# Optimization experiments

Hardware: AMD Instinct MI355X
Metric: run time of the kernel (lower is better)

Reference implementation:

```python
import jax, jax.numpy as jnp
import numpy as np

B, N, T = 8, 512, 24
HID, HOR, NID, NBLOCKS, NHIDL = 256, 24, 64, 3, 2  # block_layers=3 -> 1 input layer + 2 hidden
D = T + N * T + NID  # FcBlock input size = 12376


def div_no_nan(a, b):
    safe = jnp.where(b == 0, jnp.ones_like(b), b)
    return jnp.where(b == 0, jnp.zeros_like(a), a / safe)


def setup_inputs() -> dict:
    key = jax.random.key(0)
    ks = jax.random.split(key, 16)
    s_in = 1.0 / np.sqrt(D)
    s_h = 1.0 / np.sqrt(HID)
    return {
        "history_in": jax.random.uniform(ks[0], (B, N, T), jnp.float32),
        "node_id_in": jax.random.randint(ks[1], (B, N, 1), 0, N, dtype=jnp.int32),
        "time_of_day_in": jax.random.uniform(ks[2], (B, N, 1), jnp.float32),
        "adjacency_in": jax.random.uniform(ks[3], (B, N, N), jnp.float32),
        "node_emb": jax.random.uniform(ks[4], (N, NID), jnp.float32, -0.05, 0.05),
        "W_in": jax.random.normal(ks[5], (NBLOCKS, D, HID), jnp.float32) * s_in,
        "b_in": jnp.zeros((NBLOCKS, HID), jnp.float32),
        "W_hid": jax.random.normal(ks[6], (NBLOCKS, NHIDL, HID, HID), jnp.float32) * s_h,
        "b_hid": jnp.zeros((NBLOCKS, NHIDL, HID), jnp.float32),
        "W_f": jax.random.normal(ks[7], (NBLOCKS, HID, HOR), jnp.float32) * s_h,
        "b_f": jnp.zeros((NBLOCKS, HOR), jnp.float32),
        "W_b": jax.random.normal(ks[8], (NBLOCKS, HID, D), jnp.float32) * s_h,
        "b_b": jnp.zeros((NBLOCKS, D), jnp.float32),
    }


def fc_block(x, W_in, b_in, W_hid, b_hid, W_f, b_f, W_b, b_b):
    # x: [B, N, D]
    h = jax.nn.relu(jnp.einsum('bnd,dh->bnh', x, W_in) + b_in)
    for l in range(NHIDL):
        h = jax.nn.relu(jnp.einsum('bnh,hk->bnk', h, W_hid[l]) + b_hid[l])
    forecast = jnp.einsum('bnh,ho->bno', h, W_f) + b_f
    backcast = jax.nn.relu(x - (jnp.einsum('bnh,hd->bnd', h, W_b) + b_b))
    return backcast, forecast


def reference(history_in, node_id_in, time_of_day_in, adjacency_in, node_emb,
              W_in, b_in, W_hid, b_hid, W_f, b_f, W_b, b_b):
    # node id embedding: [B,N,1] -> [B,N,1,NID] -> squeeze -> [B,N,NID]
    node_id = node_emb[node_id_in[..., 0]]

    # use_time_gate=False: time_gate_forward = 0, time_gate_backward = 0
    # history_in = history_in / (1 + 0) -> unchanged

    # graph_layer_type == 'none' branch with graph_adj = adjacency_in [B,N,N]
    level = jnp.max(history_in, axis=-1, keepdims=True)          # [B,N,1]
    history = div_no_nan(history_in, level)                      # [B,N,T]

    # tile history to all pairs and weight by adjacency: [B,N,N,T]
    all_node_history = adjacency_in[..., None] * history_in[:, None, :, :]
    all_node_history = all_node_history.reshape(B, N, N * T)     # [B,N,N*T]
    all_node_history = div_no_nan(all_node_history - level, level)
    all_node_history = jnp.where(all_node_history > 0, all_node_history, 0.0)

    history = jnp.concatenate([history, all_node_history, node_id], axis=-1)  # [B,N,D]

    backcast, forecast_out = fc_block(history, W_in[0], b_in[0], W_hid[0], b_hid[0],
                                      W_f[0], b_f[0], W_b[0], b_b[0])
    for i in range(1, NBLOCKS):
        backcast, fb = fc_block(backcast, W_in[i], b_in[i], W_hid[i], b_hid[i],
                                W_f[i], b_f[i], W_b[i], b_b[i])
        forecast_out = forecast_out + fb

    forecast_out = forecast_out[:, :, :HOR]
    forecast = forecast_out * level  # (1 + time_gate_forward) = 1
    return backcast, forecast
```

## Files before the change

### kernel.cpp

```cpp
#include <hip/hip_runtime.h>

#define Bq   8
#define Nn   512
#define Tt   24
#define NIDc 64
#define HIDc 256
#define HORc 24
#define Dd   12376
#define Mm   4096
#define DdPad 12384
#define NbPad 12416
#define SPLITK 8
#define KCHUNK 1568

typedef float  f32x4  __attribute__((ext_vector_type(4)));
typedef short  bf16x8 __attribute__((ext_vector_type(8)));

__device__ __forceinline__ ushort f2bf(float f) {
    unsigned u = __float_as_uint(f);
    u += 0x7FFF + ((u >> 16) & 1);
    return (ushort)(u >> 16);
}
__device__ __forceinline__ float bf2f(ushort h) {
    return __uint_as_float(((unsigned)h) << 16);
}

#define ASYNC16(g, l) __builtin_amdgcn_global_load_lds(                        \
    (const __attribute__((address_space(1))) unsigned*)(g),                    \
    (__attribute__((address_space(3))) unsigned*)(l), 16, 0, 0)

__global__ __launch_bounds__(256) void build_x_kernel(
    const float* __restrict__ hist, const int* __restrict__ nid,
    const float* __restrict__ adj, const float* __restrict__ emb,
    ushort* __restrict__ x, float* __restrict__ level)
{
    int bn = blockIdx.x;
    int b  = bn >> 9;
    __shared__ float sh[Tt];
    __shared__ float slv;
    int tid = threadIdx.x;
    const float* hrow = hist + (size_t)bn * Tt;
    if (tid < Tt) sh[tid] = hrow[tid];
    __syncthreads();
    if (tid == 0) {
        float m = sh[0];
        #pragma unroll
        for (int t = 1; t < Tt; t++) m = fmaxf(m, sh[t]);
        slv = m;
        level[bn] = m;
    }
    __syncthreads();
    float lv  = slv;
    float inv = (lv == 0.0f) ? 0.0f : 1.0f / lv;
    ushort* xr = x + (size_t)bn * DdPad;
    if (tid < Tt) xr[tid] = f2bf(sh[tid] * inv);
    const float* hb   = hist + (size_t)b * Nn * Tt;
    const float* arow = adj  + (size_t)bn * Nn;
    for (int base = tid * 8; base < Nn * Tt; base += 256 * 8) {
        bf16x8 pack;
        #pragma unroll
        for (int e = 0; e < 8; e++) {
            int idx = base + e;
            int m_ = idx / Tt;
            int t  = idx - m_ * Tt;
            float v = arow[m_] * hb[m_ * Tt + t];
            float r = (v - lv) * inv;
            pack[e] = (short)f2bf((r > 0.0f) ? r : 0.0f);
        }
        *(bf16x8*)(xr + Tt + base) = pack;
    }
    if (tid < NIDc) {
        int id = nid[bn];
        xr[Tt + Nn * Tt + tid] = f2bf(emb[(size_t)id * NIDc + tid]);
    }
    if (tid < DdPad - Dd) xr[Dd + tid] = 0;
}

__global__ __launch_bounds__(256) void transpose_w(
    const float* __restrict__ W, ushort* __restrict__ Bt,
    int K, int N, int Kpad)
{
    __shared__ ushort tile[32][72];
    const int k0 = blockIdx.x * 32;
    const int n0 = blockIdx.y * 64;
    const int tid = threadIdx.x;
    #pragma unroll
    for (int i = 0; i < 8; i++) {
        const int idx = tid + i * 256;
        const int kk = idx >> 6;
        const int nn = idx & 63;
        const int gk = k0 + kk, gn = n0 + nn;
        const float v = (gk < K && gn < N) ? W[(size_t)gk * N + gn] : 0.0f;
        tile[kk][nn] = f2bf(v);
    }
    __syncthreads();
    const int n  = tid >> 2;
    const int kc = (tid & 3) << 3;
    uint4 o;
    o.x = (unsigned)tile[kc + 0][n] | ((unsigned)tile[kc + 1][n] << 16);
    o.y = (unsigned)tile[kc + 2][n] | ((unsigned)tile[kc + 3][n] << 16);
    o.z = (unsigned)tile[kc + 4][n] | ((unsigned)tile[kc + 5][n] << 16);
    o.w = (unsigned)tile[kc + 6][n] | ((unsigned)tile[kc + 7][n] << 16);
    *(uint4*)(Bt + (size_t)(n0 + n) * Kpad + k0 + kc) = o;
}

template <int TM, int TN, int EPI>
__global__ __launch_bounds__(256) void gemm_mfma(
    const ushort* __restrict__ A, int lda,
    const ushort* __restrict__ Bt, int ldbt,
    const float* __restrict__ bias,
    const ushort* __restrict__ X, int ldx,
    void* __restrict__ Cp, int ldc,
    int K, int N, int chunk)
{
    constexpr int WI = TM / 32;
    constexpr int WJ = TN / 32;
    __shared__ ushort As[TM * 32];
    __shared__ ushort Bs[TN * 32];

    const int tid  = threadIdx.x;
    const int row0 = blockIdx.x * TM;
    const int col0 = blockIdx.y * TN;
    const int spl  = blockIdx.z;
    const int kstart = spl * chunk;
    const int kend   = min(K, kstart + chunk);
    const int iters  = (kend - kstart) >> 5;

    const int lane = tid & 63;
    const int wave = tid >> 6;
    const int quad = lane >> 4;
    const int l15  = lane & 15;
    const int wm   = (wave >> 1) * (TM / 2);
    const int wn   = (wave & 1) * (TN / 2);

    f32x4 acc[WI][WJ];
    #pragma unroll
    for (int i = 0; i < WI; i++)
        #pragma unroll
        for (int j = 0; j < WJ; j++)
            acc[i][j] = (f32x4){0.f, 0.f, 0.f, 0.f};

    for (int kt = 0; kt < iters; ++kt) {
        const int kb = kstart + (kt << 5);
        #pragma unroll
        for (int s = wave; s < TM / 16; s += 4) {
            const int r = s * 16 + (lane >> 2);
            ASYNC16(A + (size_t)(row0 + r) * lda + kb + ((lane & 3) << 3),
                    As + s * 512);
        }
        #pragma unroll
        for (int s = wave; s < TN / 16; s += 4) {
            const int r = s * 16 + (lane >> 2);
            ASYNC16(Bt + (size_t)(col0 + r) * ldbt + kb + ((lane & 3) << 3),
                    Bs + s * 512);
        }
        __syncthreads();

        bf16x8 af[WI], bfr[WJ];
        #pragma unroll
        for (int i = 0; i < WI; i++)
            af[i] = *(const bf16x8*)&As[(wm + i * 16 + l15) * 32 + quad * 8];
        #pragma unroll
        for (int j = 0; j < WJ; j++)
            bfr[j] = *(const bf16x8*)&Bs[(wn + j * 16 + l15) * 32 + quad * 8];
        #pragma unroll
        for (int i = 0; i < WI; i++)
            #pragma unroll
            for (int j = 0; j < WJ; j++)
                acc[i][j] = __builtin_amdgcn_mfma_f32_16x16x32_bf16(
                    bfr[j], af[i], acc[i][j], 0, 0, 0);
        __syncthreads();
    }

    #pragma unroll
    for (int i = 0; i < WI; i++) {
        const int row = row0 + wm + i * 16 + l15;
        #pragma unroll
        for (int j = 0; j < WJ; j++) {
            const int c0 = col0 + wn + j * 16 + quad * 4;
            const f32x4 v = acc[i][j];
            if (EPI == 0) {
                *(f32x4*)&((float*)Cp)[(size_t)spl * Mm * HIDc +
                                       (size_t)row * ldc + c0] = v;
            } else if (EPI == 1) {
                const float4 bb = *(const float4*)&bias[c0];
                ushort4 o;
                o.x = f2bf(fmaxf(v[0] + bb.x, 0.f));
                o.y = f2bf(fmaxf(v[1] + bb.y, 0.f));
                o.z = f2bf(fmaxf(v[2] + bb.z, 0.f));
                o.w = f2bf(fmaxf(v[3] + bb.w, 0.f));
                *(ushort4*)&((ushort*)Cp)[(size_t)row * ldc + c0] = o;
            } else if (EPI == 2) {
                if (c0 < N) {
                    const float4 bb = *(const float4*)&bias[c0];
                    const ushort4 xq = *(const ushort4*)&X[(size_t)row * ldx + c0];
                    f32x4 o;
                    o[0] = fmaxf(bf2f(xq.x) - (v[0] + bb.x), 0.f);
                    o[1] = fmaxf(bf2f(xq.y) - (v[1] + bb.y), 0.f);
                    o[2] = fmaxf(bf2f(xq.z) - (v[2] + bb.z), 0.f);
                    o[3] = fmaxf(bf2f(xq.w) - (v[3] + bb.w), 0.f);
                    __builtin_nontemporal_store(
                        o, (f32x4*)&((float*)Cp)[(size_t)row * ldc + c0]);
                }
            } else {
                if (c0 < N) {
                    const float4 bb = *(const float4*)&bias[c0];
                    const ushort4 xq = *(const ushort4*)&X[(size_t)row * ldx + c0];
                    ushort4 o;
                    o.x = f2bf(fmaxf(bf2f(xq.x) - (v[0] + bb.x), 0.f));
                    o.y = f2bf(fmaxf(bf2f(xq.y) - (v[1] + bb.y), 0.f));
                    o.z = f2bf(fmaxf(bf2f(xq.z) - (v[2] + bb.z), 0.f));
                    o.w = f2bf(fmaxf(bf2f(xq.w) - (v[3] + bb.w), 0.f));
                    *(ushort4*)&((ushort*)Cp)[(size_t)row * ldc + c0] = o;
                }
            }
        }
    }
}

__global__ __launch_bounds__(256) void reduce_hin(
    const float* __restrict__ partial, const float* __restrict__ bias,
    ushort* __restrict__ h)
{
    const int gid = (blockIdx.x * 256 + threadIdx.x) * 4;
    f32x4 s = *(const f32x4*)&bias[gid & (HIDc - 1)];
    #pragma unroll
    for (int j = 0; j < SPLITK; j++)
        s += *(const f32x4*)&partial[(size_t)j * (Mm * HIDc) + gid];
    ushort4 o;
    o.x = f2bf(fmaxf(s[0], 0.f));
    o.y = f2bf(fmaxf(s[1], 0.f));
    o.z = f2bf(fmaxf(s[2], 0.f));
    o.w = f2bf(fmaxf(s[3], 0.f));
    *(ushort4*)&h[gid] = o;
}

__global__ __launch_bounds__(256) void gemm_forecast_kernel(
    const ushort* __restrict__ h, const float* __restrict__ Wf,
    const float* __restrict__ bf, float* __restrict__ fc, int accumulate)
{
    int gid = blockIdx.x * 256 + threadIdx.x;
    if (gid >= Mm * HORc) return;
    int row = gid / HORc;
    int col = gid - row * HORc;
    const ushort* hr = h + (size_t)row * HIDc;
    float acc = 0.0f;
    #pragma unroll 4
    for (int k = 0; k < HIDc; k++)
        acc = fmaf(bf2f(hr[k]), Wf[k * HORc + col], acc);
    acc += bf[col];
    if (accumulate) fc[gid] += acc;
    else            fc[gid]  = acc;
}

__global__ __launch_bounds__(256) void finalize_kernel(
    const float* __restrict__ fc, const float* __restrict__ level,
    float* __restrict__ out)
{
    int gid = blockIdx.x * 256 + threadIdx.x;
    if (gid >= Mm * HORc) return;
    out[gid] = fc[gid] * level[gid / HORc];
}

extern "C" void kernel_launch(void* const* d_in, const int* in_sizes, int n_in,
                              void* d_out, int out_size, void* d_ws, size_t ws_size,
                              hipStream_t stream)
{
    const float* hist  = (const float*)d_in[0];
    const int*   nid   = (const int*)  d_in[1];
    const float* adj   = (const float*)d_in[3];
    const float* emb   = (const float*)d_in[4];
    const float* W_in  = (const float*)d_in[5];
    const float* b_in  = (const float*)d_in[6];
    const float* W_hid = (const float*)d_in[7];
    const float* b_hid = (const float*)d_in[8];
    const float* W_f   = (const float*)d_in[9];
    const float* b_f   = (const float*)d_in[10];
    const float* W_b   = (const float*)d_in[11];
    const float* b_b   = (const float*)d_in[12];

    float* bout = (float*)d_out;
    float* fout = (float*)d_out + (size_t)Mm * Dd;

    char* ws = (char*)d_ws;
    size_t off = 0;
    float*  level = (float*) (ws + off); off += 16384;
    float*  fc    = (float*) (ws + off); off += (size_t)Mm * HORc * 4;
    ushort* hA    = (ushort*)(ws + off); off += (size_t)Mm * HIDc * 2;
    ushort* hB    = (ushort*)(ws + off); off += (size_t)Mm * HIDc * 2;
    ushort* WtIn  = (ushort*)(ws + off); off += (size_t)3 * HIDc * DdPad * 2;
    ushort* WtHid = (ushort*)(ws + off); off += (size_t)6 * HIDc * HIDc * 2;
    ushort* WtB   = (ushort*)(ws + off); off += (size_t)3 * NbPad * HIDc * 2;
    float*  part  = (float*) (ws + off); off += (size_t)SPLITK * Mm * HIDc * 4;
    ushort* xb    = (ushort*)(ws + off); off += (size_t)Mm * DdPad * 2;

    build_x_kernel<<<Mm, 256, 0, stream>>>(hist, nid, adj, emb, xb, level);

    for (int i = 0; i < 3; i++)
        transpose_w<<<dim3(DdPad / 32, HIDc / 64), 256, 0, stream>>>(
            W_in + (size_t)i * Dd * HIDc, WtIn + (size_t)i * HIDc * DdPad,
            Dd, HIDc, DdPad);
    for (int l = 0; l < 6; l++)
        transpose_w<<<dim3(HIDc / 32, HIDc / 64), 256, 0, stream>>>(
            W_hid + (size_t)l * HIDc * HIDc, WtHid + (size_t)l * HIDc * HIDc,
            HIDc, HIDc, HIDc);
    for (int i = 0; i < 3; i++)
        transpose_w<<<dim3(HIDc / 32, NbPad / 64), 256, 0, stream>>>(
            W_b + (size_t)i * HIDc * Dd, WtB + (size_t)i * NbPad * HIDc,
            HIDc, Dd, HIDc);

    for (int i = 0; i < 3; i++) {
        const float* bi  = b_in  + (size_t)i * HIDc;
        const float* bh0 = b_hid + (size_t)(i * 2 + 0) * HIDc;
        const float* bh1 = b_hid + (size_t)(i * 2 + 1) * HIDc;
        const float* Wfi = W_f   + (size_t)i * HIDc * HORc;
        const float* bfi = b_f   + (size_t)i * HORc;
        const float* bbi = b_b   + (size_t)i * Dd;

        gemm_mfma<128, 128, 0>
            <<<dim3(Mm / 128, HIDc / 128, SPLITK), 256, 0, stream>>>(
            xb, DdPad, WtIn + (size_t)i * HIDc * DdPad, DdPad,
            nullptr, nullptr, 0, part, HIDc, DdPad, HIDc, KCHUNK);
        reduce_hin<<<Mm * HIDc / 1024, 256, 0, stream>>>(part, bi, hA);

        gemm_mfma<64, 64, 1>
            <<<dim3(Mm / 64, HIDc / 64, 1), 256, 0, stream>>>(
            hA, HIDc, WtHid + (size_t)(2 * i) * HIDc * HIDc, HIDc,
            bh0, nullptr, 0, hB, HIDc, HIDc, HIDc, HIDc);
        gemm_mfma<64, 64, 1>
            <<<dim3(Mm / 64, HIDc / 64, 1), 256, 0, stream>>>(
            hB, HIDc, WtHid + (size_t)(2 * i + 1) * HIDc * HIDc, HIDc,
            bh1, nullptr, 0, hA, HIDc, HIDc, HIDc, HIDc);

        gemm_forecast_kernel<<<(Mm * HORc + 255) / 256, 256, 0, stream>>>(
            hA, Wfi, bfi, fc, i > 0 ? 1 : 0);

        if (i < 2) {
            gemm_mfma<128, 128, 3>
                <<<dim3(Mm / 128, NbPad / 128, 1), 256, 0, stream>>>(
                hA, HIDc, WtB + (size_t)i * NbPad * HIDc, HIDc,
                bbi, xb, DdPad, xb, DdPad, HIDc, Dd, HIDc);
        } else {
            gemm_mfma<128, 128, 2>
                <<<dim3(Mm / 128, NbPad / 128, 1), 256, 0, stream>>>(
                hA, HIDc, WtB + (size_t)i * NbPad * HIDc, HIDc,
                bbi, xb, DdPad, bout, Dd, HIDc, Dd, HIDc);
        }
    }

    finalize_kernel<<<(Mm * HORc + 255) / 256, 256, 0, stream>>>(fc, level, fout);
}
```

Measured before the change: 935.1 us.

## Double-buffer LDS tiles in MFMA GEMM, prefetch epilogue operands, shrink hidden tiles

Shared-memory A/B tiles are double-buffered: the next K-slice is loaded asynchronously while MFMAs run on the current one. Explicit vmcnt waits and raw s_barriers replace the two __syncthreads per iteration. Bias and residual X values for the epilogue are loaded before the main loop, so their latency overlaps the K loop, at the cost of extra registers. The hidden-layer GEMMs switch from 64x64 to 32x32 tiles for more blocks, and the final backcast store no longer uses a nontemporal hint.

```diff
diff --git a/kernel.cpp b/kernel.cpp
--- a/kernel.cpp
+++ b/kernel.cpp
@@ -115,8 +115,13 @@
 {
     constexpr int WI = TM / 32;
     constexpr int WJ = TN / 32;
-    __shared__ ushort As[TM * 32];
-    __shared__ ushort Bs[TN * 32];
+    constexpr int SA = TM / 16;
+    constexpr int SB = TN / 16;
+    constexpr int LPW = (SA + SB) / 4;
+    static_assert((SA + SB) % 4 == 0, "uniform loads per wave required");
+    static_assert(LPW == 1 || LPW == 2 || LPW == 4, "vmcnt literal");
+    __shared__ ushort As[2][TM * 32];
+    __shared__ ushort Bs[2][TN * 32];
 
     const int tid  = threadIdx.x;
     const int row0 = blockIdx.x * TM;
@@ -140,36 +145,85 @@
         for (int j = 0; j < WJ; j++)
             acc[i][j] = (f32x4){0.f, 0.f, 0.f, 0.f};
 
+    auto stage = [&](int buf, int kb) {
+        #pragma unroll
+        for (int t = 0; t < LPW; t++) {
+            const int s = wave + 4 * t;
+            if (s < SA) {
+                const int r = s * 16 + (lane >> 2);
+                ASYNC16(A + (size_t)(row0 + r) * lda + kb + ((lane & 3) << 3),
+                        &As[buf][s * 512]);
+            } else {
+                const int s2 = s - SA;
+                const int r = s2 * 16 + (lane >> 2);
+                ASYNC16(Bt + (size_t)(col0 + r) * ldbt + kb + ((lane & 3) << 3),
+                        &Bs[buf][s2 * 512]);
+            }
+        }
+    };
+
+    stage(0, kstart);
+
+    float4  bpre[WJ];
+    ushort4 xpre[WI][WJ];
+    bool    cok[WJ];
+    #pragma unroll
+    for (int j = 0; j < WJ; j++) {
+        const int c0 = col0 + wn + j * 16 + quad * 4;
+        cok[j] = (c0 < N);
+        if constexpr (EPI == 1) {
+            bpre[j] = *(const float4*)&bias[c0];
+        } else if constexpr (EPI >= 2) {
+            bpre[j] = cok[j] ? *(const float4*)&bias[c0]
+                             : float4{0.f, 0.f, 0.f, 0.f};
+        }
+    }
+    if constexpr (EPI >= 2) {
+        #pragma unroll
+        for (int i = 0; i < WI; i++) {
+            const int row = row0 + wm + i * 16 + l15;
+            #pragma unroll
+            for (int j = 0; j < WJ; j++) {
+                const int c0 = col0 + wn + j * 16 + quad * 4;
+                xpre[i][j] = cok[j]
+                    ? *(const ushort4*)&X[(size_t)row * ldx + c0]
+                    : ushort4{0, 0, 0, 0};
+            }
+        }
+    }
+
     for (int kt = 0; kt < iters; ++kt) {
-        const int kb = kstart + (kt << 5);
-        #pragma unroll
-        for (int s = wave; s < TM / 16; s += 4) {
-            const int r = s * 16 + (lane >> 2);
-            ASYNC16(A + (size_t)(row0 + r) * lda + kb + ((lane & 3) << 3),
-                    As + s * 512);
-        }
-        #pragma unroll
-        for (int s = wave; s < TN / 16; s += 4) {
-            const int r = s * 16 + (lane >> 2);
-            ASYNC16(Bt + (size_t)(col0 + r) * ldbt + kb + ((lane & 3) << 3),
-                    Bs + s * 512);
-        }
-        __syncthreads();
+        const int cur = kt & 1;
+        if (kt + 1 < iters) {
+            stage(cur ^ 1, kstart + ((kt + 1) << 5));
+            if constexpr (LPW == 4)
+                asm volatile("s_waitcnt vmcnt(4)" ::: "memory");
+            else if constexpr (LPW == 2)
+                asm volatile("s_waitcnt vmcnt(2)" ::: "memory");
+            else
+                asm volatile("s_waitcnt vmcnt(1)" ::: "memory");
+        } else {
+            asm volatile("s_waitcnt vmcnt(0)" ::: "memory");
+        }
+        __builtin_amdgcn_s_barrier();
+        __builtin_amdgcn_sched_barrier(0);
 
         bf16x8 af[WI], bfr[WJ];
         #pragma unroll
         for (int i = 0; i < WI; i++)
-            af[i] = *(const bf16x8*)&As[(wm + i * 16 + l15) * 32 + quad * 8];
+            af[i] = *(const bf16x8*)&As[cur][(wm + i * 16 + l15) * 32 + quad * 8];
         #pragma unroll
         for (int j = 0; j < WJ; j++)
-            bfr[j] = *(const bf16x8*)&Bs[(wn + j * 16 + l15) * 32 + quad * 8];
+            bfr[j] = *(const bf16x8*)&Bs[cur][(wn + j * 16 + l15) * 32 + quad * 8];
         #pragma unroll
         for (int i = 0; i < WI; i++)
             #pragma unroll
             for (int j = 0; j < WJ; j++)
                 acc[i][j] = __builtin_amdgcn_mfma_f32_16x16x32_bf16(
                     bfr[j], af[i], acc[i][j], 0, 0, 0);
-        __syncthreads();
+
+        __builtin_amdgcn_sched_barrier(0);
+        __builtin_amdgcn_s_barrier();
     }
 
     #pragma unroll
@@ -179,38 +233,32 @@
         for (int j = 0; j < WJ; j++) {
             const int c0 = col0 + wn + j * 16 + quad * 4;
             const f32x4 v = acc[i][j];
-            if (EPI == 0) {
+            if constexpr (EPI == 0) {
                 *(f32x4*)&((float*)Cp)[(size_t)spl * Mm * HIDc +
                                        (size_t)row * ldc + c0] = v;
-            } else if (EPI == 1) {
-                const float4 bb = *(const float4*)&bias[c0];
+            } else if constexpr (EPI == 1) {
                 ushort4 o;
-                o.x = f2bf(fmaxf(v[0] + bb.x, 0.f));
-                o.y = f2bf(fmaxf(v[1] + bb.y, 0.f));
-                o.z = f2bf(fmaxf(v[2] + bb.z, 0.f));
-                o.w = f2bf(fmaxf(v[3] + bb.w, 0.f));
+                o.x = f2bf(fmaxf(v[0] + bpre[j].x, 0.f));
+                o.y = f2bf(fmaxf(v[1] + bpre[j].y, 0.f));
+                o.z = f2bf(fmaxf(v[2] + bpre[j].z, 0.f));
+                o.w = f2bf(fmaxf(v[3] + bpre[j].w, 0.f));
                 *(ushort4*)&((ushort*)Cp)[(size_t)row * ldc + c0] = o;
-            } else if (EPI == 2) {
-                if (c0 < N) {
-                    const float4 bb = *(const float4*)&bias[c0];
-                    const ushort4 xq = *(const ushort4*)&X[(size_t)row * ldx + c0];
+            } else if constexpr (EPI == 2) {
+                if (cok[j]) {
                     f32x4 o;
-                    o[0] = fmaxf(bf2f(xq.x) - (v[0] + bb.x), 0.f);
-                    o[1] = fmaxf(bf2f(xq.y) - (v[1] + bb.y), 0.f);
-                    o[2] = fmaxf(bf2f(xq.z) - (v[2] + bb.z), 0.f);
-                    o[3] = fmaxf(bf2f(xq.w) - (v[3] + bb.w), 0.f);
-                    __builtin_nontemporal_store(
-                        o, (f32x4*)&((float*)Cp)[(size_t)row * ldc + c0]);
+                    o[0] = fmaxf(bf2f(xpre[i][j].x) - (v[0] + bpre[j].x), 0.f);
+                    o[1] = fmaxf(bf2f(xpre[i][j].y) - (v[1] + bpre[j].y), 0.f);
+                    o[2] = fmaxf(bf2f(xpre[i][j].z) - (v[2] + bpre[j].z), 0.f);
+                    o[3] = fmaxf(bf2f(xpre[i][j].w) - (v[3] + bpre[j].w), 0.f);
+                    *(f32x4*)&((float*)Cp)[(size_t)row * ldc + c0] = o;
                 }
             } else {
-                if (c0 < N) {
-                    const float4 bb = *(const float4*)&bias[c0];
-                    const ushort4 xq = *(const ushort4*)&X[(size_t)row * ldx + c0];
+                if (cok[j]) {
                     ushort4 o;
-                    o.x = f2bf(fmaxf(bf2f(xq.x) - (v[0] + bb.x), 0.f));
-                    o.y = f2bf(fmaxf(bf2f(xq.y) - (v[1] + bb.y), 0.f));
-                    o.z = f2bf(fmaxf(bf2f(xq.z) - (v[2] + bb.z), 0.f));
-                    o.w = f2bf(fmaxf(bf2f(xq.w) - (v[3] + bb.w), 0.f));
+                    o.x = f2bf(fmaxf(bf2f(xpre[i][j].x) - (v[0] + bpre[j].x), 0.f));
+                    o.y = f2bf(fmaxf(bf2f(xpre[i][j].y) - (v[1] + bpre[j].y), 0.f));
+                    o.z = f2bf(fmaxf(bf2f(xpre[i][j].z) - (v[2] + bpre[j].z), 0.f));
+                    o.w = f2bf(fmaxf(bf2f(xpre[i][j].w) - (v[3] + bpre[j].w), 0.f));
                     *(ushort4*)&((ushort*)Cp)[(size_t)row * ldc + c0] = o;
                 }
             }
@@ -323,12 +371,12 @@
             nullptr, nullptr, 0, part, HIDc, DdPad, HIDc, KCHUNK);
         reduce_hin<<<Mm * HIDc / 1024, 256, 0, stream>>>(part, bi, hA);
 
-        gemm_mfma<64, 64, 1>
-            <<<dim3(Mm / 64, HIDc / 64, 1), 256, 0, stream>>>(
+        gemm_mfma<32, 32, 1>
+            <<<dim3(Mm / 32, HIDc / 32, 1), 256, 0, stream>>>(
             hA, HIDc, WtHid + (size_t)(2 * i) * HIDc * HIDc, HIDc,
             bh0, nullptr, 0, hB, HIDc, HIDc, HIDc, HIDc);
-        gemm_mfma<64, 64, 1>
-            <<<dim3(Mm / 64, HIDc / 64, 1), 256, 0, stream>>>(
+        gemm_mfma<32, 32, 1>
+            <<<dim3(Mm / 32, HIDc / 32, 1), 256, 0, stream>>>(
             hB, HIDc, WtHid + (size_t)(2 * i + 1) * HIDc * HIDc, HIDc,
             bh1, nullptr, 0, hA, HIDc, HIDc, HIDc, HIDc);
 
```

Result: faster. 891.6 us (-4.6%).
